# Kernel optimization log

Hardware: AMD Instinct MI355X
Metric: run time of the kernel (lower is better)

## Reference

```python
import jax, jax.numpy as jnp
import numpy as np

N, K, D_IN, D_H, D_A, N_CLS = 8192, 10, 1024, 512, 256, 4


def setup_inputs() -> dict:
    key = jax.random.key(0)
    ks = jax.random.split(key, 20)
    def lin(k, fan_in, shape):
        return jax.random.normal(k, shape, dtype=jnp.float32) / np.sqrt(fan_in)
    return {
        "x_path": jax.random.normal(ks[0], (N, D_IN), dtype=jnp.float32),
        "cluster_id": jax.random.randint(ks[1], (N,), 0, K),
        # per-cluster phi MLP (Linear 1024->512, ReLU, Linear 512->512, ReLU); dropout = eval identity
        "W1": lin(ks[2], D_IN, (K, D_IN, D_H)), "b1": jnp.zeros((K, D_H), jnp.float32),
        "W2": lin(ks[3], D_H, (K, D_H, D_H)), "b2": jnp.zeros((K, D_H), jnp.float32),
        # attention_net fc: Linear 512->512 + ReLU
        "fc_W": lin(ks[4], D_H, (D_H, D_H)), "fc_b": jnp.zeros((D_H,), jnp.float32),
        # Attn_Net_Gated: a=tanh(Va), b=sigmoid(Vb), A=(a*b)@Vc
        "Va": lin(ks[5], D_H, (D_H, D_A)), "ba": jnp.zeros((D_A,), jnp.float32),
        "Vb": lin(ks[6], D_H, (D_H, D_A)), "bb": jnp.zeros((D_A,), jnp.float32),
        "Vc": lin(ks[7], D_A, (D_A, 1)), "bc": jnp.zeros((1,), jnp.float32),
        # rho: Linear 512->256 + ReLU
        "rho_W": lin(ks[8], D_H, (D_H, D_A)), "rho_b": jnp.zeros((D_A,), jnp.float32),
        # classifier: Linear 256->4
        "cls_W": lin(ks[9], D_A, (D_A, N_CLS)), "cls_b": jnp.zeros((N_CLS,), jnp.float32),
    }


def reference(x_path, cluster_id, W1, b1, W2, b2, fc_W, fc_b,
              Va, ba, Vb, bb, Vc, bc, rho_W, rho_b, cls_W, cls_b):
    # mask[k, n] = 1 if patch n belongs to cluster k
    mask = (cluster_id[None, :] == jnp.arange(K)[:, None]).astype(x_path.dtype)  # [K, N]

    # per-cluster 2-layer MLP applied to all patches, masked mean-pool (= AdaptiveAvgPool1d(1))
    def phi(W1i, b1i, W2i, b2i):
        h = jax.nn.relu(x_path @ W1i + b1i)          # [N, 512]
        return jax.nn.relu(h @ W2i + b2i)            # [N, 512]
    y = jax.vmap(phi)(W1, b1, W2, b2)                # [K, N, 512]
    cnt = mask.sum(axis=1)                           # [K]
    pooled = jnp.einsum('kn,knd->kd', mask, y) / jnp.maximum(cnt, 1.0)[:, None]  # [K, 512]
    # empty cluster -> zeros (matches torch.zeros((1,512)) branch since b terms are zero via where)
    pooled = jnp.where(cnt[:, None] > 0, pooled, 0.0)

    # attention_net: fc + gated attention
    h = jax.nn.relu(pooled @ fc_W + fc_b)            # [K, 512]
    a = jnp.tanh(h @ Va + ba)                        # [K, 256]
    b = jax.nn.sigmoid(h @ Vb + bb)                  # [K, 256]
    A = (a * b) @ Vc + bc                            # [K, 1]
    A = jax.nn.softmax(A.T, axis=1)                  # [1, K]
    h_path = A @ h                                   # [1, 512]
    h_path = jax.nn.relu(h_path @ rho_W + rho_b)[0]  # [256]
    logits = (h_path @ cls_W + cls_b)[None, :]       # [1, 4]
    Y_hat = jnp.argmax(logits, axis=1, keepdims=True)
    hazards = jax.nn.sigmoid(logits)
    S = jnp.cumprod(1.0 - hazards, axis=1)
    return hazards, S, Y_hat
```

## Files before the change

kernel.cpp:

```cpp
#include <hip/hip_runtime.h>
#include <math.h>

#define NPATCH 8192
#define KC     10
#define DIN    1024
#define DH     512
#define DA     256
#define NCLS   4

typedef unsigned short u16;
typedef short bf16x8 __attribute__((ext_vector_type(8)));
typedef float f32x4  __attribute__((ext_vector_type(4)));

#define OFF_CNT   0
#define OFF_BAR   48
#define OFF_IDX   64
#define OFF_PSUM  327744
#define OFF_H     348224
#define OFF_H2    368768
#define OFF_SRED  369792
#define OFF_W1P   373888
#define OFF_W2P   10859648
#define OFF_XC    16102528
#define OFF_H1    32879744

__device__ __forceinline__ u16 f2bf(float f) {
  union { float f; unsigned u; } v; v.f = f;
  unsigned r = (v.u + 0x7fffu + ((v.u >> 16) & 1u)) >> 16;
  return (u16)r;
}

struct __align__(8) U16x4 { u16 x, y, z, w; };

__device__ __forceinline__ void dma16(const u16* gp, u16* lp) {
  __builtin_amdgcn_global_load_lds(
      (const __attribute__((address_space(1))) void*)gp,
      (__attribute__((address_space(3))) void*)lp, 16, 0, 0);
}

#define W1_TILES (KC * (DIN / 32) * (DH / 32))
#define W2_TILES (KC * (DH / 32) * (DH / 32))
#define NB_BUCKET 32
#define WT_PER_BLK 4
#define NB_PREP (NB_BUCKET + (W1_TILES + W2_TILES) / WT_PER_BLK)

__global__ __launch_bounds__(256) void prep_kernel(
    const int* __restrict__ cid, int* __restrict__ cnt,
    int* __restrict__ idxlist, const float* __restrict__ W1,
    const float* __restrict__ W2, u16* __restrict__ W1p,
    u16* __restrict__ W2p, float* __restrict__ psum) {
  int b = blockIdx.x, t = threadIdx.x;
  if (b < NB_BUCKET) {
    int g = b * 256 + t;
    if (g < KC * DH) psum[g] = 0.f;
    __shared__ int lcnt[KC], lbase[KC];
    if (t < KC) lcnt[t] = 0;
    __syncthreads();
    int n = b * 256 + t;
    int k = cid[n];
    int myoff = atomicAdd(&lcnt[k], 1);
    __syncthreads();
    if (t < KC) lbase[t] = atomicAdd(&cnt[t], lcnt[t]);
    __syncthreads();
    idxlist[k * NPATCH + lbase[k] + myoff] = n;
  } else {
    __shared__ u16 tile[32][33];
#pragma unroll
    for (int it = 0; it < WT_PER_BLK; ++it) {
      int bb = (b - NB_BUCKET) * WT_PER_BLK + it;
      const float* src;
      u16* dst;
      if (bb < W1_TILES) {
        int k = bb / 512, rem = bb % 512;
        int kb = rem / 16, n0 = (rem % 16) * 32;
        src = W1 + (size_t)k * DIN * DH + (size_t)kb * 32 * DH + n0;
        dst = W1p + (((size_t)(k * 32 + kb) * 512 + n0) * 32);
      } else {
        int b2 = bb - W1_TILES;
        int k = b2 / 256, rem = b2 % 256;
        int kb = rem / 16, n0 = (rem % 16) * 32;
        src = W2 + (size_t)k * DH * DH + (size_t)kb * 32 * DH + n0;
        dst = W2p + (((size_t)(k * 16 + kb) * 512 + n0) * 32);
      }
      {
        int ki = t >> 3, n4 = (t & 7) * 4;
        float4 v = *(const float4*)&src[(size_t)ki * DH + n4];
        tile[ki][n4 + 0] = f2bf(v.x);
        tile[ki][n4 + 1] = f2bf(v.y);
        tile[ki][n4 + 2] = f2bf(v.z);
        tile[ki][n4 + 3] = f2bf(v.w);
      }
      __syncthreads();
      {
        int n = t >> 3, ki = (t & 7) * 4;
        U16x4 o = {tile[ki + 0][n], tile[ki + 1][n], tile[ki + 2][n],
                   tile[ki + 3][n]};
        int kis = ki ^ (((n >> 1) & 3) << 3);
        *(U16x4*)&dst[(size_t)n * 32 + kis] = o;
      }
      __syncthreads();
    }
  }
}

__global__ __launch_bounds__(256) void pack_kernel(
    const float* __restrict__ x, const int* __restrict__ cnt,
    const int* __restrict__ idxlist, u16* __restrict__ xc) {
  const int b = blockIdx.x, t = threadIdx.x;
  int cb[KC];
  {
    int a = 0;
#pragma unroll
    for (int i = 0; i < KC; ++i) { cb[i] = a; a += cnt[i]; }
  }
  int row = b * 32 + (t >> 3);
  int k = 0;
#pragma unroll
  for (int i = 1; i < KC; ++i) k = (row >= cb[i]) ? i : k;
  int src = idxlist[k * NPATCH + (row - cb[k])];
  const float4* xp = (const float4*)(x + (size_t)src * DIN + (t & 7) * 128);
  U16x4* dst = (U16x4*)(xc + (size_t)row * DIN + (t & 7) * 128);
#pragma unroll
  for (int j = 0; j < 32; ++j) {
    float4 v = xp[j];
    U16x4 o = {f2bf(v.x), f2bf(v.y), f2bf(v.z), f2bf(v.w)};
    dst[j] = o;
  }
}


__global__ __launch_bounds__(256, 2) void phi1_kernel(
    const u16* __restrict__ xc, const u16* __restrict__ W1p,
    const float* __restrict__ b1, const int* __restrict__ cnt,
    u16* __restrict__ h1) {
  const int slice = blockIdx.x, k = blockIdx.y, chunk = blockIdx.z;
  const int cntk = cnt[k];
  const int row0 = chunk * 128;
  if (row0 >= cntk) return;
  int cbase = 0;
#pragma unroll
  for (int i = 0; i < KC - 1; ++i) cbase += (i < k) ? cnt[i] : 0;

  const int tid = threadIdx.x;
  const int w = tid >> 6, lane = tid & 63;
  const int quad = lane >> 4, l16 = lane & 15;
  const int wr = w >> 1, wc = w & 1;
  const int rl = lane >> 2, gl = lane & 3;

  __shared__ __align__(16) u16 lds[17408];
  u16* As = lds;
  u16* Bs = lds + 8192;

  const size_t arow0 = (size_t)(cbase + row0);

#pragma unroll
  for (int jj = 0; jj < 2; ++jj) {
    int rg = w * 2 + jj;
    int row_l = rg * 16 + rl;
    size_t grow = arow0 + row_l; if (grow > 8191) grow = 8191;
    int g = gl ^ ((row_l >> 1) & 3);
    dma16(xc + grow * DIN + g * 8, As + rg * 512);
  }
#pragma unroll
  for (int jj = 0; jj < 2; ++jj) {
    int cg = w * 2 + jj;
    int col_l = cg * 16 + rl;
    dma16(W1p + ((size_t)(k * 32) * 512 + slice * 128 + col_l) * 32 + gl * 8,
          Bs + cg * 512);
  }

  const f32x4 zero4 = {0.f, 0.f, 0.f, 0.f};
  f32x4 acc[4][4];
#pragma unroll
  for (int fr = 0; fr < 4; ++fr)
#pragma unroll
    for (int fc = 0; fc < 4; ++fc) acc[fr][fc] = zero4;

  for (int t = 0; t < 32; ++t) {
    const int buf = t & 1;
    if (t < 31) {
      const int tn = t + 1, bn = buf ^ 1;
#pragma unroll
      for (int jj = 0; jj < 2; ++jj) {
        int rg = w * 2 + jj;
        int row_l = rg * 16 + rl;
        size_t grow = arow0 + row_l; if (grow > 8191) grow = 8191;
        int g = gl ^ ((row_l >> 1) & 3);
        dma16(xc + grow * DIN + tn * 32 + g * 8, As + bn * 4096 + rg * 512);
      }
#pragma unroll
      for (int jj = 0; jj < 2; ++jj) {
        int cg = w * 2 + jj;
        int col_l = cg * 16 + rl;
        dma16(W1p + ((size_t)(k * 32 + tn) * 512 + slice * 128 + col_l) * 32 +
                  gl * 8,
              Bs + bn * 4096 + cg * 512);
      }
      asm volatile("s_waitcnt vmcnt(4)" ::: "memory");
    } else {
      asm volatile("s_waitcnt vmcnt(0)" ::: "memory");
    }
    __syncthreads();
    bf16x8 af[4], bfr[4];
#pragma unroll
    for (int fr = 0; fr < 4; ++fr) {
      int row = wr * 64 + fr * 16 + l16;
      af[fr] = *(const bf16x8*)&As[buf * 4096 + row * 32 +
                                   ((quad ^ ((row >> 1) & 3)) << 3)];
    }
#pragma unroll
    for (int fc = 0; fc < 4; ++fc) {
      int col = wc * 64 + fc * 16 + l16;
      bfr[fc] = *(const bf16x8*)&Bs[buf * 4096 + col * 32 +
                                    ((quad ^ ((col >> 1) & 3)) << 3)];
    }
#pragma unroll
    for (int fr = 0; fr < 4; ++fr)
#pragma unroll
      for (int fc = 0; fc < 4; ++fc)
        acc[fr][fc] = __builtin_amdgcn_mfma_f32_16x16x32_bf16(
            af[fr], bfr[fc], acc[fr][fc], 0, 0, 0);
    __syncthreads();
  }

#pragma unroll
  for (int fr = 0; fr < 4; ++fr)
#pragma unroll
    for (int fc = 0; fc < 4; ++fc) {
      int col = wc * 64 + fc * 16 + l16;
      float bias = b1[k * DH + slice * 128 + col];
#pragma unroll
      for (int r = 0; r < 4; ++r) {
        int row = wr * 64 + fr * 16 + quad * 4 + r;
        lds[row * 136 + col] = f2bf(fmaxf(acc[fr][fc][r] + bias, 0.f));
      }
    }
  __syncthreads();
  {
    int row = tid >> 1, half = tid & 1;
    if (row0 + row < cntk) {
      u16* dst = h1 + (arow0 + row) * DH + slice * 128 + half * 64;
      const u16* srcl = &lds[row * 136 + half * 64];
#pragma unroll
      for (int j = 0; j < 8; ++j)
        *(bf16x8*)(dst + j * 8) = *(const bf16x8*)(srcl + j * 8);
    }
  }
}

__global__ __launch_bounds__(256, 2) void phi2_kernel(
    const u16* __restrict__ h1, const u16* __restrict__ W2p,
    const float* __restrict__ b2, const int* __restrict__ cnt,
    float* __restrict__ psum) {
  const int slice = blockIdx.x, k = blockIdx.y, chunk = blockIdx.z;
  const int cntk = cnt[k];
  const int row0 = chunk * 128;
  if (row0 >= cntk) return;
  int cbase = 0;
#pragma unroll
  for (int i = 0; i < KC - 1; ++i) cbase += (i < k) ? cnt[i] : 0;

  const int tid = threadIdx.x;
  const int w = tid >> 6, lane = tid & 63;
  const int quad = lane >> 4, l16 = lane & 15;
  const int wr = w >> 1, wc = w & 1;
  const int rl = lane >> 2, gl = lane & 3;

  __shared__ __align__(16) u16 lds[16384];
  u16* As = lds;
  u16* Bs = lds + 8192;

  const size_t arow0 = (size_t)(cbase + row0);

#pragma unroll
  for (int jj = 0; jj < 2; ++jj) {
    int rg = w * 2 + jj;
    int row_l = rg * 16 + rl;
    size_t grow = arow0 + row_l; if (grow > 8191) grow = 8191;
    int g = gl ^ ((row_l >> 1) & 3);
    dma16(h1 + grow * DH + g * 8, As + rg * 512);
  }
#pragma unroll
  for (int jj = 0; jj < 2; ++jj) {
    int cg = w * 2 + jj;
    int col_l = cg * 16 + rl;
    dma16(W2p + ((size_t)(k * 16) * 512 + slice * 128 + col_l) * 32 + gl * 8,
          Bs + cg * 512);
  }

  const f32x4 zero4 = {0.f, 0.f, 0.f, 0.f};
  f32x4 acc[4][4];
#pragma unroll
  for (int fr = 0; fr < 4; ++fr)
#pragma unroll
    for (int fc = 0; fc < 4; ++fc) acc[fr][fc] = zero4;

  for (int t = 0; t < 16; ++t) {
    const int buf = t & 1;
    if (t < 15) {
      const int tn = t + 1, bn = buf ^ 1;
#pragma unroll
      for (int jj = 0; jj < 2; ++jj) {
        int rg = w * 2 + jj;
        int row_l = rg * 16 + rl;
        size_t grow = arow0 + row_l; if (grow > 8191) grow = 8191;
        int g = gl ^ ((row_l >> 1) & 3);
        dma16(h1 + grow * DH + tn * 32 + g * 8, As + bn * 4096 + rg * 512);
      }
#pragma unroll
      for (int jj = 0; jj < 2; ++jj) {
        int cg = w * 2 + jj;
        int col_l = cg * 16 + rl;
        dma16(W2p + ((size_t)(k * 16 + tn) * 512 + slice * 128 + col_l) * 32 +
                  gl * 8,
              Bs + bn * 4096 + cg * 512);
      }
      asm volatile("s_waitcnt vmcnt(4)" ::: "memory");
    } else {
      asm volatile("s_waitcnt vmcnt(0)" ::: "memory");
    }
    __syncthreads();
    bf16x8 af[4], bfr[4];
#pragma unroll
    for (int fr = 0; fr < 4; ++fr) {
      int row = wr * 64 + fr * 16 + l16;
      af[fr] = *(const bf16x8*)&As[buf * 4096 + row * 32 +
                                   ((quad ^ ((row >> 1) & 3)) << 3)];
    }
#pragma unroll
    for (int fc = 0; fc < 4; ++fc) {
      int col = wc * 64 + fc * 16 + l16;
      bfr[fc] = *(const bf16x8*)&Bs[buf * 4096 + col * 32 +
                                    ((quad ^ ((col >> 1) & 3)) << 3)];
    }
#pragma unroll
    for (int fr = 0; fr < 4; ++fr)
#pragma unroll
      for (int fc = 0; fc < 4; ++fc)
        acc[fr][fc] = __builtin_amdgcn_mfma_f32_16x16x32_bf16(
            af[fr], bfr[fc], acc[fr][fc], 0, 0, 0);
    __syncthreads();
  }

#pragma unroll
  for (int fc = 0; fc < 4; ++fc) {
    int col = wc * 64 + fc * 16 + l16;
    float bias = b2[k * DH + slice * 128 + col];
    float sv = 0.f;
#pragma unroll
    for (int fr = 0; fr < 4; ++fr)
#pragma unroll
      for (int r = 0; r < 4; ++r) {
        int row = row0 + wr * 64 + fr * 16 + quad * 4 + r;
        sv += (row < cntk) ? fmaxf(acc[fr][fc][r] + bias, 0.f) : 0.f;
      }
    sv += __shfl_xor(sv, 16, 64);
    sv += __shfl_xor(sv, 32, 64);
    if (quad == 0) atomicAdd(&psum[k * DH + slice * 128 + col], sv);
  }
}

#define NTB 64

__device__ __forceinline__ void bar_arrive_wait(int* bar) {
  __syncthreads();
  if (threadIdx.x == 0) {
    __threadfence();
    __hip_atomic_fetch_add(bar, 1, __ATOMIC_RELEASE, __HIP_MEMORY_SCOPE_AGENT);
    while (__hip_atomic_load(bar, __ATOMIC_ACQUIRE,
                             __HIP_MEMORY_SCOPE_AGENT) < NTB) {
      __builtin_amdgcn_s_sleep(1);
    }
  }
  __syncthreads();
}

__global__ __launch_bounds__(256) void tail_kernel(
    const float* __restrict__ psum, const int* __restrict__ cnt,
    const float* __restrict__ fcW, const float* __restrict__ fcb,
    const float* __restrict__ Va, const float* __restrict__ ba,
    const float* __restrict__ Vb, const float* __restrict__ bb_,
    const float* __restrict__ Vc, const float* __restrict__ rhoW,
    const float* __restrict__ rhob, const float* __restrict__ clsW,
    const float* __restrict__ clsb, float* __restrict__ hstore,
    float* __restrict__ sred, float* __restrict__ h2g,
    int* __restrict__ bar, float* __restrict__ out) {
  __shared__ float p_sh[KC * DH];
  __shared__ float r1[2560];
  __shared__ float r2[2560];
  __shared__ float invs[KC];
  __shared__ float gate_sh[4 * KC];
  __shared__ float ws_sh[KC];
  __shared__ float hp_sh[DH];
  const int tid = threadIdx.x;
  const int b = blockIdx.x;

  if (tid < KC) {
    int c = cnt[tid];
    invs[tid] = (c > 0) ? 1.f / (float)c : 0.f;
  }
  __syncthreads();
#pragma unroll
  for (int it = 0; it < KC * DH / 256; ++it) {
    int e = it * 256 + tid;
    p_sh[e] = psum[e] * invs[e >> 9];
  }
  __syncthreads();
  {
    const int jj = tid & 7, dq = tid >> 3;
    const int j0 = b * 8;
    float acc[KC];
#pragma unroll
    for (int k = 0; k < KC; ++k) acc[k] = 0.f;
#pragma unroll 4
    for (int i = 0; i < 16; ++i) {
      int d = dq * 16 + i;
      float wv = fcW[(size_t)d * DH + j0 + jj];
#pragma unroll
      for (int k = 0; k < KC; ++k) acc[k] = fmaf(p_sh[k * DH + d], wv, acc[k]);
    }
#pragma unroll
    for (int k = 0; k < KC; ++k) r1[(dq * 8 + jj) * KC + k] = acc[k];
    __syncthreads();
    if (tid < 8 * KC) {
      int jj2 = tid / KC, k = tid % KC;
      float s = 0.f;
#pragma unroll
      for (int q = 0; q < 32; ++q) s += r1[(q * 8 + jj2) * KC + k];
      hstore[k * DH + j0 + jj2] = fmaxf(s + fcb[j0 + jj2], 0.f);
    }
  }
  bar_arrive_wait(&bar[0]);

#pragma unroll
  for (int it = 0; it < KC * DH / 256; ++it) {
    int e = it * 256 + tid;
    p_sh[e] = hstore[e];
  }
  __syncthreads();
  {
    const int jj = tid & 3, dq = tid >> 2;
    const int j0 = b * 4;
    float sa[KC], sb[KC];
#pragma unroll
    for (int k = 0; k < KC; ++k) { sa[k] = 0.f; sb[k] = 0.f; }
#pragma unroll 4
    for (int i = 0; i < 8; ++i) {
      int d = dq * 8 + i;
      float va = Va[(size_t)d * DA + j0 + jj];
      float vb = Vb[(size_t)d * DA + j0 + jj];
#pragma unroll
      for (int k = 0; k < KC; ++k) {
        float h = p_sh[k * DH + d];
        sa[k] = fmaf(h, va, sa[k]);
        sb[k] = fmaf(h, vb, sb[k]);
      }
    }
#pragma unroll
    for (int k = 0; k < KC; ++k) {
      r1[(dq * 4 + jj) * KC + k] = sa[k];
      r2[(dq * 4 + jj) * KC + k] = sb[k];
    }
    __syncthreads();
    if (tid < 4 * KC) {
      int jj2 = tid / KC, k = tid % KC;
      float ta = 0.f, tb = 0.f;
#pragma unroll
      for (int q = 0; q < 64; ++q) {
        ta += r1[(q * 4 + jj2) * KC + k];
        tb += r2[(q * 4 + jj2) * KC + k];
      }
      float a = tanhf(ta + ba[j0 + jj2]);
      float g = 1.f / (1.f + expf(-(tb + bb_[j0 + jj2])));
      gate_sh[jj2 * KC + k] = a * g * Vc[j0 + jj2];
    }
    __syncthreads();
    if (tid < KC) {
      float s = 0.f;
#pragma unroll
      for (int jj2 = 0; jj2 < 4; ++jj2) s += gate_sh[jj2 * KC + tid];
      sred[b * 16 + tid] = s;
    }
  }
  bar_arrive_wait(&bar[1]);

  if (tid < KC) {
    float s = 0.f;
    for (int q = 0; q < NTB; ++q) s += sred[q * 16 + tid];
    ws_sh[tid] = s;
  }
  __syncthreads();
  if (tid == 0) {
    float m = -1e30f;
#pragma unroll
    for (int k2 = 0; k2 < KC; ++k2) m = fmaxf(m, ws_sh[k2]);
    float Z = 0.f;
#pragma unroll
    for (int k2 = 0; k2 < KC; ++k2) {
      float e = expf(ws_sh[k2] - m);
      ws_sh[k2] = e;
      Z += e;
    }
    float iZ = 1.f / Z;
#pragma unroll
    for (int k2 = 0; k2 < KC; ++k2) ws_sh[k2] *= iZ;
  }
  __syncthreads();
#pragma unroll
  for (int it = 0; it < 2; ++it) {
    int d = it * 256 + tid;
    float s = 0.f;
#pragma unroll
    for (int k2 = 0; k2 < KC; ++k2) s = fmaf(ws_sh[k2], p_sh[k2 * DH + d], s);
    hp_sh[d] = s;
  }
  __syncthreads();
  {
    const int jj = tid & 3, dq = tid >> 2;
    const int j0 = b * 4;
    float acc = 0.f;
#pragma unroll 4
    for (int i = 0; i < 8; ++i) {
      int d = dq * 8 + i;
      acc = fmaf(hp_sh[d], rhoW[(size_t)d * DA + j0 + jj], acc);
    }
    r1[dq * 4 + jj] = acc;
    __syncthreads();
    if (tid < 4) {
      float s = 0.f;
#pragma unroll
      for (int q = 0; q < 64; ++q) s += r1[q * 4 + tid];
      h2g[j0 + tid] = fmaxf(s + rhob[j0 + tid], 0.f);
    }
  }

  if (b != 0) {
    __syncthreads();
    if (tid == 0) {
      __threadfence();
      __hip_atomic_fetch_add(&bar[2], 1, __ATOMIC_RELEASE,
                             __HIP_MEMORY_SCOPE_AGENT);
    }
    return;
  }
  bar_arrive_wait(&bar[2]);
  {
    float h = h2g[tid];
#pragma unroll
    for (int c = 0; c < NCLS; ++c)
      r1[c * 256 + tid] = h * clsW[(size_t)tid * NCLS + c];
    __syncthreads();
    for (int s = 128; s > 0; s >>= 1) {
      if (tid < s) {
#pragma unroll
        for (int c = 0; c < NCLS; ++c)
          r1[c * 256 + tid] += r1[c * 256 + tid + s];
      }
      __syncthreads();
    }
    if (tid == 0) {
      float lg[NCLS], hz[NCLS];
      int best = 0;
#pragma unroll
      for (int c = 0; c < NCLS; ++c) {
        lg[c] = r1[c * 256] + clsb[c];
        hz[c] = 1.f / (1.f + expf(-lg[c]));
        if (lg[c] > lg[best]) best = c;
      }
      float S = 1.f;
#pragma unroll
      for (int c = 0; c < NCLS; ++c) out[c] = hz[c];
#pragma unroll
      for (int c = 0; c < NCLS; ++c) {
        S *= (1.f - hz[c]);
        out[NCLS + c] = S;
      }
      out[2 * NCLS] = (float)best;
    }
  }
}

extern "C" void kernel_launch(void* const* d_in, const int* in_sizes, int n_in,
                              void* d_out, int out_size, void* d_ws,
                              size_t ws_size, hipStream_t stream) {
  const float* x    = (const float*)d_in[0];
  const int*   cid  = (const int*)d_in[1];
  const float* W1   = (const float*)d_in[2];
  const float* b1   = (const float*)d_in[3];
  const float* W2   = (const float*)d_in[4];
  const float* b2   = (const float*)d_in[5];
  const float* fcW  = (const float*)d_in[6];
  const float* fcb  = (const float*)d_in[7];
  const float* Va   = (const float*)d_in[8];
  const float* ba   = (const float*)d_in[9];
  const float* Vb   = (const float*)d_in[10];
  const float* bb_  = (const float*)d_in[11];
  const float* Vc   = (const float*)d_in[12];
  const float* rhoW = (const float*)d_in[14];
  const float* rhob = (const float*)d_in[15];
  const float* clsW = (const float*)d_in[16];
  const float* clsb = (const float*)d_in[17];
  float* out = (float*)d_out;

  char* ws = (char*)d_ws;
  int*   cnt     = (int*)(ws + OFF_CNT);
  int*   bar     = (int*)(ws + OFF_BAR);
  int*   idxlist = (int*)(ws + OFF_IDX);
  float* psum    = (float*)(ws + OFF_PSUM);
  float* hstore  = (float*)(ws + OFF_H);
  float* h2g     = (float*)(ws + OFF_H2);
  float* sred    = (float*)(ws + OFF_SRED);
  u16*   W1p     = (u16*)(ws + OFF_W1P);
  u16*   W2p     = (u16*)(ws + OFF_W2P);
  u16*   xc      = (u16*)(ws + OFF_XC);
  u16*   h1      = (u16*)(ws + OFF_H1);

  (void)hipMemsetAsync(cnt, 0, 64, stream);
  prep_kernel<<<NB_PREP, 256, 0, stream>>>(cid, cnt, idxlist, W1, W2, W1p, W2p,
                                           psum);
  pack_kernel<<<NPATCH / 32, 256, 0, stream>>>(x, cnt, idxlist, xc);
  phi1_kernel<<<dim3(4, KC, 64), 256, 0, stream>>>(xc, W1p, b1, cnt, h1);
  phi2_kernel<<<dim3(4, KC, 64), 256, 0, stream>>>(h1, W2p, b2, cnt, psum);
  tail_kernel<<<NTB, 256, 0, stream>>>(psum, cnt, fcW, fcb, Va, ba, Vb, bb_,
                                       Vc, rhoW, rhob, clsW, clsb, hstore,
                                       sred, h2g, bar, out);
}
```

Measured before the change: 211.5 us.

## Fold x conversion into prep, gather rows via index list, use 256-row tiles

Removes the separate pack kernel. x is now converted to bf16 in original row order inside prep_kernel, and phi1/phi2 gather rows through idxlist instead of reading a cluster-sorted copy. h1 is scattered back to each patch's original row. The GEMM kernels move to 512 threads and 256-row tiles, so each W tile is loaded once per two 128-row subtiles, and the epilogue is staged through LDS in two halves. This saves one launch and a full pass over x, and halves B-operand traffic per row. In exchange, A loads become per-row gathers and LDS use per block rises, which may lower occupancy.

```diff
diff --git a/kernel.cpp b/kernel.cpp
--- a/kernel.cpp
+++ b/kernel.cpp
@@ -41,14 +41,16 @@
 #define W1_TILES (KC * (DIN / 32) * (DH / 32))
 #define W2_TILES (KC * (DH / 32) * (DH / 32))
 #define NB_BUCKET 32
+#define NB_XCONV  256
 #define WT_PER_BLK 4
-#define NB_PREP (NB_BUCKET + (W1_TILES + W2_TILES) / WT_PER_BLK)
+#define NB_PREP (NB_BUCKET + NB_XCONV + (W1_TILES + W2_TILES) / WT_PER_BLK)
 
 __global__ __launch_bounds__(256) void prep_kernel(
     const int* __restrict__ cid, int* __restrict__ cnt,
     int* __restrict__ idxlist, const float* __restrict__ W1,
     const float* __restrict__ W2, u16* __restrict__ W1p,
-    u16* __restrict__ W2p, float* __restrict__ psum) {
+    u16* __restrict__ W2p, const float* __restrict__ x,
+    u16* __restrict__ xc, float* __restrict__ psum) {
   int b = blockIdx.x, t = threadIdx.x;
   if (b < NB_BUCKET) {
     int g = b * 256 + t;
@@ -63,11 +65,21 @@
     if (t < KC) lbase[t] = atomicAdd(&cnt[t], lcnt[t]);
     __syncthreads();
     idxlist[k * NPATCH + lbase[k] + myoff] = n;
+  } else if (b < NB_BUCKET + NB_XCONV) {
+    int n = (b - NB_BUCKET) * 32 + (t >> 3);
+    const float4* xp = (const float4*)(x + (size_t)n * DIN + (t & 7) * 128);
+    U16x4* dst = (U16x4*)(xc + (size_t)n * DIN + (t & 7) * 128);
+#pragma unroll
+    for (int j = 0; j < 32; ++j) {
+      float4 v = xp[j];
+      U16x4 o = {f2bf(v.x), f2bf(v.y), f2bf(v.z), f2bf(v.w)};
+      dst[j] = o;
+    }
   } else {
     __shared__ u16 tile[32][33];
 #pragma unroll
     for (int it = 0; it < WT_PER_BLK; ++it) {
-      int bb = (b - NB_BUCKET) * WT_PER_BLK + it;
+      int bb = (b - NB_BUCKET - NB_XCONV) * WT_PER_BLK + it;
       const float* src;
       u16* dst;
       if (bb < W1_TILES) {
@@ -103,71 +115,42 @@
   }
 }
 
-__global__ __launch_bounds__(256) void pack_kernel(
-    const float* __restrict__ x, const int* __restrict__ cnt,
-    const int* __restrict__ idxlist, u16* __restrict__ xc) {
-  const int b = blockIdx.x, t = threadIdx.x;
-  int cb[KC];
-  {
-    int a = 0;
-#pragma unroll
-    for (int i = 0; i < KC; ++i) { cb[i] = a; a += cnt[i]; }
-  }
-  int row = b * 32 + (t >> 3);
-  int k = 0;
-#pragma unroll
-  for (int i = 1; i < KC; ++i) k = (row >= cb[i]) ? i : k;
-  int src = idxlist[k * NPATCH + (row - cb[k])];
-  const float4* xp = (const float4*)(x + (size_t)src * DIN + (t & 7) * 128);
-  U16x4* dst = (U16x4*)(xc + (size_t)row * DIN + (t & 7) * 128);
-#pragma unroll
-  for (int j = 0; j < 32; ++j) {
-    float4 v = xp[j];
-    U16x4 o = {f2bf(v.x), f2bf(v.y), f2bf(v.z), f2bf(v.w)};
-    dst[j] = o;
-  }
-}
-
-
-__global__ __launch_bounds__(256, 2) void phi1_kernel(
+
+__global__ __launch_bounds__(512, 2) void phi1_kernel(
     const u16* __restrict__ xc, const u16* __restrict__ W1p,
     const float* __restrict__ b1, const int* __restrict__ cnt,
-    u16* __restrict__ h1) {
+    const int* __restrict__ idxlist, u16* __restrict__ h1) {
   const int slice = blockIdx.x, k = blockIdx.y, chunk = blockIdx.z;
   const int cntk = cnt[k];
-  const int row0 = chunk * 128;
-  if (row0 >= cntk) return;
-  int cbase = 0;
-#pragma unroll
-  for (int i = 0; i < KC - 1; ++i) cbase += (i < k) ? cnt[i] : 0;
+  const int base = chunk * 256;
+  if (base >= cntk) return;
 
   const int tid = threadIdx.x;
   const int w = tid >> 6, lane = tid & 63;
   const int quad = lane >> 4, l16 = lane & 15;
   const int wr = w >> 1, wc = w & 1;
   const int rl = lane >> 2, gl = lane & 3;
-
-  __shared__ __align__(16) u16 lds[17408];
+  const int gsw = gl ^ ((rl >> 1) & 3);
+  const int rsw = (quad ^ ((l16 >> 1) & 3)) << 3;
+
+  __shared__ __align__(16) u16 lds[24576];
   u16* As = lds;
-  u16* Bs = lds + 8192;
-
-  const size_t arow0 = (size_t)(cbase + row0);
-
+  u16* Bs = lds + 16384;
+
+  int ridx[2];
 #pragma unroll
   for (int jj = 0; jj < 2; ++jj) {
-    int rg = w * 2 + jj;
-    int row_l = rg * 16 + rl;
-    size_t grow = arow0 + row_l; if (grow > 8191) grow = 8191;
-    int g = gl ^ ((row_l >> 1) & 3);
-    dma16(xc + grow * DIN + g * 8, As + rg * 512);
-  }
-#pragma unroll
-  for (int jj = 0; jj < 2; ++jj) {
-    int cg = w * 2 + jj;
-    int col_l = cg * 16 + rl;
-    dma16(W1p + ((size_t)(k * 32) * 512 + slice * 128 + col_l) * 32 + gl * 8,
-          Bs + cg * 512);
-  }
+    int row_l = (w * 2 + jj) * 16 + rl;
+    ridx[jj] = (base + row_l < cntk) ? idxlist[k * NPATCH + base + row_l] : 0;
+  }
+  const u16* bsrc =
+      W1p + ((size_t)(k * 32) * 512 + slice * 128 + w * 16 + rl) * 32 + gl * 8;
+
+#pragma unroll
+  for (int jj = 0; jj < 2; ++jj)
+    dma16(xc + (size_t)ridx[jj] * DIN + gsw * 8,
+          As + (w * 2 + jj) * 512);
+  dma16(bsrc, Bs + w * 512);
 
   const f32x4 zero4 = {0.f, 0.f, 0.f, 0.f};
   f32x4 acc[4][4];
@@ -179,24 +162,13 @@
   for (int t = 0; t < 32; ++t) {
     const int buf = t & 1;
     if (t < 31) {
-      const int tn = t + 1, bn = buf ^ 1;
-#pragma unroll
-      for (int jj = 0; jj < 2; ++jj) {
-        int rg = w * 2 + jj;
-        int row_l = rg * 16 + rl;
-        size_t grow = arow0 + row_l; if (grow > 8191) grow = 8191;
-        int g = gl ^ ((row_l >> 1) & 3);
-        dma16(xc + grow * DIN + tn * 32 + g * 8, As + bn * 4096 + rg * 512);
-      }
-#pragma unroll
-      for (int jj = 0; jj < 2; ++jj) {
-        int cg = w * 2 + jj;
-        int col_l = cg * 16 + rl;
-        dma16(W1p + ((size_t)(k * 32 + tn) * 512 + slice * 128 + col_l) * 32 +
-                  gl * 8,
-              Bs + bn * 4096 + cg * 512);
-      }
-      asm volatile("s_waitcnt vmcnt(4)" ::: "memory");
+      const int bn = buf ^ 1, tn = t + 1;
+#pragma unroll
+      for (int jj = 0; jj < 2; ++jj)
+        dma16(xc + (size_t)ridx[jj] * DIN + tn * 32 + gsw * 8,
+              As + bn * 8192 + (w * 2 + jj) * 512);
+      dma16(bsrc + (size_t)tn * 16384, Bs + bn * 4096 + w * 512);
+      asm volatile("s_waitcnt vmcnt(3)" ::: "memory");
     } else {
       asm volatile("s_waitcnt vmcnt(0)" ::: "memory");
     }
@@ -205,14 +177,12 @@
 #pragma unroll
     for (int fr = 0; fr < 4; ++fr) {
       int row = wr * 64 + fr * 16 + l16;
-      af[fr] = *(const bf16x8*)&As[buf * 4096 + row * 32 +
-                                   ((quad ^ ((row >> 1) & 3)) << 3)];
+      af[fr] = *(const bf16x8*)&As[buf * 8192 + row * 32 + rsw];
     }
 #pragma unroll
     for (int fc = 0; fc < 4; ++fc) {
       int col = wc * 64 + fc * 16 + l16;
-      bfr[fc] = *(const bf16x8*)&Bs[buf * 4096 + col * 32 +
-                                    ((quad ^ ((col >> 1) & 3)) << 3)];
+      bfr[fc] = *(const bf16x8*)&Bs[buf * 4096 + col * 32 + rsw];
     }
 #pragma unroll
     for (int fr = 0; fr < 4; ++fr)
@@ -224,69 +194,72 @@
   }
 
 #pragma unroll
-  for (int fr = 0; fr < 4; ++fr)
-#pragma unroll
-    for (int fc = 0; fc < 4; ++fc) {
-      int col = wc * 64 + fc * 16 + l16;
-      float bias = b1[k * DH + slice * 128 + col];
-#pragma unroll
-      for (int r = 0; r < 4; ++r) {
-        int row = wr * 64 + fr * 16 + quad * 4 + r;
-        lds[row * 136 + col] = f2bf(fmaxf(acc[fr][fc][r] + bias, 0.f));
-      }
-    }
-  __syncthreads();
-  {
-    int row = tid >> 1, half = tid & 1;
-    if (row0 + row < cntk) {
-      u16* dst = h1 + (arow0 + row) * DH + slice * 128 + half * 64;
-      const u16* srcl = &lds[row * 136 + half * 64];
-#pragma unroll
-      for (int j = 0; j < 8; ++j)
-        *(bf16x8*)(dst + j * 8) = *(const bf16x8*)(srcl + j * 8);
-    }
-  }
-}
-
-__global__ __launch_bounds__(256, 2) void phi2_kernel(
+  for (int half = 0; half < 2; ++half) {
+    __syncthreads();
+    if ((wr >> 1) == half) {
+#pragma unroll
+      for (int fr = 0; fr < 4; ++fr)
+#pragma unroll
+        for (int fc = 0; fc < 4; ++fc) {
+          int col = wc * 64 + fc * 16 + l16;
+          float bias = b1[k * DH + slice * 128 + col];
+#pragma unroll
+          for (int r = 0; r < 4; ++r) {
+            int lrow = (wr & 1) * 64 + fr * 16 + quad * 4 + r;
+            lds[lrow * 136 + col] = f2bf(fmaxf(acc[fr][fc][r] + bias, 0.f));
+          }
+        }
+    }
+    __syncthreads();
+    {
+      int lrow = tid >> 2, seg = tid & 3;
+      int brow = base + half * 128 + lrow;
+      if (brow < cntk) {
+        int n = idxlist[k * NPATCH + brow];
+        u16* dst = h1 + (size_t)n * DH + slice * 128 + seg * 32;
+#pragma unroll
+        for (int j = 0; j < 4; ++j)
+          *(bf16x8*)(dst + j * 8) =
+              *(const bf16x8*)&lds[lrow * 136 + seg * 32 + j * 8];
+      }
+    }
+  }
+}
+
+__global__ __launch_bounds__(512, 2) void phi2_kernel(
     const u16* __restrict__ h1, const u16* __restrict__ W2p,
     const float* __restrict__ b2, const int* __restrict__ cnt,
-    float* __restrict__ psum) {
+    const int* __restrict__ idxlist, float* __restrict__ psum) {
   const int slice = blockIdx.x, k = blockIdx.y, chunk = blockIdx.z;
   const int cntk = cnt[k];
-  const int row0 = chunk * 128;
-  if (row0 >= cntk) return;
-  int cbase = 0;
-#pragma unroll
-  for (int i = 0; i < KC - 1; ++i) cbase += (i < k) ? cnt[i] : 0;
+  const int base = chunk * 256;
+  if (base >= cntk) return;
 
   const int tid = threadIdx.x;
   const int w = tid >> 6, lane = tid & 63;
   const int quad = lane >> 4, l16 = lane & 15;
   const int wr = w >> 1, wc = w & 1;
   const int rl = lane >> 2, gl = lane & 3;
-
-  __shared__ __align__(16) u16 lds[16384];
+  const int gsw = gl ^ ((rl >> 1) & 3);
+  const int rsw = (quad ^ ((l16 >> 1) & 3)) << 3;
+
+  __shared__ __align__(16) u16 lds[24576];
   u16* As = lds;
-  u16* Bs = lds + 8192;
-
-  const size_t arow0 = (size_t)(cbase + row0);
-
+  u16* Bs = lds + 16384;
+
+  int ridx[2];
 #pragma unroll
   for (int jj = 0; jj < 2; ++jj) {
-    int rg = w * 2 + jj;
-    int row_l = rg * 16 + rl;
-    size_t grow = arow0 + row_l; if (grow > 8191) grow = 8191;
-    int g = gl ^ ((row_l >> 1) & 3);
-    dma16(h1 + grow * DH + g * 8, As + rg * 512);
-  }
-#pragma unroll
-  for (int jj = 0; jj < 2; ++jj) {
-    int cg = w * 2 + jj;
-    int col_l = cg * 16 + rl;
-    dma16(W2p + ((size_t)(k * 16) * 512 + slice * 128 + col_l) * 32 + gl * 8,
-          Bs + cg * 512);
-  }
+    int row_l = (w * 2 + jj) * 16 + rl;
+    ridx[jj] = (base + row_l < cntk) ? idxlist[k * NPATCH + base + row_l] : 0;
+  }
+  const u16* bsrc =
+      W2p + ((size_t)(k * 16) * 512 + slice * 128 + w * 16 + rl) * 32 + gl * 8;
+
+#pragma unroll
+  for (int jj = 0; jj < 2; ++jj)
+    dma16(h1 + (size_t)ridx[jj] * DH + gsw * 8, As + (w * 2 + jj) * 512);
+  dma16(bsrc, Bs + w * 512);
 
   const f32x4 zero4 = {0.f, 0.f, 0.f, 0.f};
   f32x4 acc[4][4];
@@ -298,24 +271,13 @@
   for (int t = 0; t < 16; ++t) {
     const int buf = t & 1;
     if (t < 15) {
-      const int tn = t + 1, bn = buf ^ 1;
-#pragma unroll
-      for (int jj = 0; jj < 2; ++jj) {
-        int rg = w * 2 + jj;
-        int row_l = rg * 16 + rl;
-        size_t grow = arow0 + row_l; if (grow > 8191) grow = 8191;
-        int g = gl ^ ((row_l >> 1) & 3);
-        dma16(h1 + grow * DH + tn * 32 + g * 8, As + bn * 4096 + rg * 512);
-      }
-#pragma unroll
-      for (int jj = 0; jj < 2; ++jj) {
-        int cg = w * 2 + jj;
-        int col_l = cg * 16 + rl;
-        dma16(W2p + ((size_t)(k * 16 + tn) * 512 + slice * 128 + col_l) * 32 +
-                  gl * 8,
-              Bs + bn * 4096 + cg * 512);
-      }
-      asm volatile("s_waitcnt vmcnt(4)" ::: "memory");
+      const int bn = buf ^ 1, tn = t + 1;
+#pragma unroll
+      for (int jj = 0; jj < 2; ++jj)
+        dma16(h1 + (size_t)ridx[jj] * DH + tn * 32 + gsw * 8,
+              As + bn * 8192 + (w * 2 + jj) * 512);
+      dma16(bsrc + (size_t)tn * 16384, Bs + bn * 4096 + w * 512);
+      asm volatile("s_waitcnt vmcnt(3)" ::: "memory");
     } else {
       asm volatile("s_waitcnt vmcnt(0)" ::: "memory");
     }
@@ -324,14 +286,12 @@
 #pragma unroll
     for (int fr = 0; fr < 4; ++fr) {
       int row = wr * 64 + fr * 16 + l16;
-      af[fr] = *(const bf16x8*)&As[buf * 4096 + row * 32 +
-                                   ((quad ^ ((row >> 1) & 3)) << 3)];
+      af[fr] = *(const bf16x8*)&As[buf * 8192 + row * 32 + rsw];
     }
 #pragma unroll
     for (int fc = 0; fc < 4; ++fc) {
       int col = wc * 64 + fc * 16 + l16;
-      bfr[fc] = *(const bf16x8*)&Bs[buf * 4096 + col * 32 +
-                                    ((quad ^ ((col >> 1) & 3)) << 3)];
+      bfr[fc] = *(const bf16x8*)&Bs[buf * 4096 + col * 32 + rsw];
     }
 #pragma unroll
     for (int fr = 0; fr < 4; ++fr)
@@ -351,7 +311,7 @@
     for (int fr = 0; fr < 4; ++fr)
 #pragma unroll
       for (int r = 0; r < 4; ++r) {
-        int row = row0 + wr * 64 + fr * 16 + quad * 4 + r;
+        int row = base + wr * 64 + fr * 16 + quad * 4 + r;
         sv += (row < cntk) ? fmaxf(acc[fr][fc][r] + bias, 0.f) : 0.f;
       }
     sv += __shfl_xor(sv, 16, 64);
@@ -617,10 +577,11 @@
 
   (void)hipMemsetAsync(cnt, 0, 64, stream);
   prep_kernel<<<NB_PREP, 256, 0, stream>>>(cid, cnt, idxlist, W1, W2, W1p, W2p,
-                                           psum);
-  pack_kernel<<<NPATCH / 32, 256, 0, stream>>>(x, cnt, idxlist, xc);
-  phi1_kernel<<<dim3(4, KC, 64), 256, 0, stream>>>(xc, W1p, b1, cnt, h1);
-  phi2_kernel<<<dim3(4, KC, 64), 256, 0, stream>>>(h1, W2p, b2, cnt, psum);
+                                           x, xc, psum);
+  phi1_kernel<<<dim3(4, KC, 32), 512, 0, stream>>>(xc, W1p, b1, cnt, idxlist,
+                                                   h1);
+  phi2_kernel<<<dim3(4, KC, 32), 512, 0, stream>>>(h1, W2p, b2, cnt, idxlist,
+                                                   psum);
   tail_kernel<<<NTB, 256, 0, stream>>>(psum, cnt, fcW, fcb, Va, ba, Vb, bb_,
                                        Vc, rhoW, rhob, clsW, clsb, hstore,
                                        sred, h2g, bar, out);
```

Result: slower. 220.5 us (+4.2%).
